# Kernel tuning notes

Measured on AMD Instinct MI355X. Metric: run time of the kernel, lower is better.

The kernel has to match this reference:

```python
import jax, jax.numpy as jnp
import numpy as np

B, S, HIDDEN = 1, 2048, 2048
HEADS, HEAD_DIM = 32, 128
EPS = 1e-5
THETA = 10000.0


def setup_inputs() -> dict:
    key = jax.random.key(0)
    k0, k1, k2 = jax.random.split(key, 3)
    hidden_states = jax.random.normal(k0, (B, S, HIDDEN), jnp.float32)
    positions = jnp.broadcast_to(jnp.arange(S, dtype=jnp.int32)[None, :], (B, S))
    qkv_w = jax.random.normal(k1, (3 * HEADS * HEAD_DIM, HIDDEN), jnp.float32) * 0.02
    q_norm_w = jnp.ones((HEAD_DIM,), jnp.float32)
    k_norm_w = jnp.ones((HEAD_DIM,), jnp.float32)
    o_proj_w = jax.random.normal(k2, (HIDDEN, HEADS * HEAD_DIM), jnp.float32) * 0.02
    return {"hidden_states": hidden_states, "positions": positions, "qkv_w": qkv_w,
            "q_norm_w": q_norm_w, "k_norm_w": k_norm_w, "o_proj_w": o_proj_w}


def _rmsnorm(x, w):
    # RMSNorm over last (head_dim) axis
    var = jnp.mean(x * x, axis=-1, keepdims=True)
    return x * jax.lax.rsqrt(var + EPS) * w


def _rope(x, positions):
    # NeoX-style (non-interleaved) rotary over full head_dim
    d2 = HEAD_DIM // 2
    inv_freq = 1.0 / (THETA ** (jnp.arange(0, HEAD_DIM, 2, dtype=jnp.float32) / HEAD_DIM))
    freqs = positions.astype(jnp.float32)[..., None] * inv_freq  # [B,S,d2]
    cos = jnp.cos(freqs)[:, :, None, :]  # [B,S,1,d2]
    sin = jnp.sin(freqs)[:, :, None, :]
    x1, x2 = x[..., :d2], x[..., d2:]
    return jnp.concatenate([x1 * cos - x2 * sin, x2 * cos + x1 * sin], axis=-1)


def reference(hidden_states, positions, qkv_w, q_norm_w, k_norm_w, o_proj_w):
    b, s, _ = hidden_states.shape
    qkv = jnp.einsum('bsh,oh->bso', hidden_states, qkv_w)  # [B,S,3*H*D]
    q, k, v = jnp.split(qkv, 3, axis=-1)
    q = q.reshape(b, s, HEADS, HEAD_DIM)
    k = k.reshape(b, s, HEADS, HEAD_DIM)
    v = v.reshape(b, s, HEADS, HEAD_DIM)
    # qk_norm (per-head RMSNorm)
    q = _rmsnorm(q, q_norm_w)
    k = _rmsnorm(k, k_norm_w)
    # rotary embedding
    q = _rope(q, positions)
    k = _rope(k, positions)
    # causal attention, scale = head_dim**-0.5 (flash_attn default)
    scale = HEAD_DIM ** -0.5
    scores = jnp.einsum('bqhd,bkhd->bhqk', q, k) * scale  # [B,H,S,S]
    causal = jnp.tril(jnp.ones((s, s), dtype=bool))
    scores = jnp.where(causal[None, None], scores, jnp.float32(-1e30))
    probs = jax.nn.softmax(scores, axis=-1)
    o = jnp.einsum('bhqk,bkhd->bqhd', probs, v).reshape(b, s, HEADS * HEAD_DIM)
    return jnp.einsum('bso,ho->bsh', o, o_proj_w)
```

## Files before the change

### kernel.cpp

```cpp
#include <hip/hip_runtime.h>
#include <cstdint>
#include <cstddef>

static constexpr int S_LEN = 2048;
static constexpr int HID   = 2048;
static constexpr int NH    = 32;
static constexpr int HD    = 128;
static constexpr int OD    = 4096;
static constexpr int QKV_O = 12288;

#define AS1 __attribute__((address_space(1)))
#define AS3 __attribute__((address_space(3)))

typedef __attribute__((ext_vector_type(8))) short bf16x8;
typedef __attribute__((ext_vector_type(4))) float f32x4;
typedef __attribute__((ext_vector_type(4))) short s16x4;

template <int V> struct IC { static constexpr int v = V; };

__device__ __forceinline__ short f2bf(float f) {
  unsigned u = __float_as_uint(f);
  unsigned r = (u + 0x7fffu + ((u >> 16) & 1u)) >> 16;
  return (short)r;
}
__device__ __forceinline__ float bf2f(short s) {
  return __uint_as_float(((unsigned)(unsigned short)s) << 16);
}
__device__ __forceinline__ unsigned pk2bf(float a, float b) {
  return __builtin_amdgcn_perm(__float_as_uint(b), __float_as_uint(a), 0x07060302u);
}

__global__ void convert2_kernel(const float* __restrict__ in1, short* __restrict__ out1, int n1_4,
                                const float* __restrict__ in2, short* __restrict__ out2, int n2_4) {
  int i = blockIdx.x * blockDim.x + threadIdx.x;
  const float* in; short* out; int j;
  if (i < n1_4) { in = in1; out = out1; j = i; }
  else { j = i - n1_4; if (j >= n2_4) return; in = in2; out = out2; }
  float4 f = ((const float4*)in)[j];
  s16x4 s;
  s.x = f2bf(f.x); s.y = f2bf(f.y); s.z = f2bf(f.z); s.w = f2bf(f.w);
  ((s16x4*)out)[j] = s;
}

__global__ __launch_bounds__(512, 2) void gemm128x256_bf16(
    const short* __restrict__ A, const short* __restrict__ Bw, short* __restrict__ C,
    int K, int N, int ldc) {
  __shared__ short Al[2][128 * 64];
  __shared__ short Bl[2][2][128 * 64];
  const int tid  = threadIdx.x;
  const int lane = tid & 63;
  const int quad = lane >> 4;
  const int col  = lane & 15;
  const int wave = tid >> 6;
  const int wm   = wave >> 2;
  const int wn   = wave & 3;

  const int cpx = gridDim.x >> 3;
  const int bid = blockIdx.x;
  const int swz = (bid & 7) * cpx + (bid >> 3);
  const int nbn = N >> 8;
  const int m0  = (swz / nbn) * 128;
  const int n0  = (swz % nbn) * 256;

  const int NT = K >> 6;

  f32x4 acc[4][4] = {};
  bf16x8 a[4][2], b0[2][2], b1[2][2];

  auto stA = [&](int t, int buf) {
#pragma unroll
    for (int r = 0; r < 2; ++r) {
      int idx = r * 512 + tid;
      int row = idx >> 3;
      int g   = idx & 7;
      int gs  = g ^ ((row >> 1) & 7);
      const short* ga = A + (size_t)(m0 + row) * K + t * 64 + gs * 8;
      __builtin_amdgcn_global_load_lds((const AS1 unsigned*)ga,
                                       (AS3 unsigned*)&Al[buf][idx * 8], 16, 0, 0);
    }
  };
  auto stB = [&](int t, int buf, int h) {
#pragma unroll
    for (int r = 0; r < 2; ++r) {
      int idx = r * 512 + tid;
      int row = idx >> 3;
      int g   = idx & 7;
      int gs  = g ^ ((row >> 1) & 7);
      const short* gb = Bw + (size_t)(n0 + h * 128 + row) * K + t * 64 + gs * 8;
      __builtin_amdgcn_global_load_lds((const AS1 unsigned*)gb,
                                       (AS3 unsigned*)&Bl[buf][h][idx * 8], 16, 0, 0);
    }
  };
  auto rdA = [&](int buf, int mh) {
#pragma unroll
    for (int i = 0; i < 2; ++i) {
      int rh = wm * 64 + (mh * 2 + i) * 16 + col;
#pragma unroll
      for (int kf = 0; kf < 2; ++kf)
        a[mh * 2 + i][kf] =
            *(const bf16x8*)&Al[buf][rh * 64 + (((kf * 4 + quad) ^ ((rh >> 1) & 7)) * 8)];
    }
  };
  auto rdB = [&](int buf, int nh, bf16x8 (&bb)[2][2]) {
#pragma unroll
    for (int j = 0; j < 2; ++j) {
      int br = wn * 64 + nh * 32 + j * 16 + col;
      int bh = br >> 7, rh = br & 127;
#pragma unroll
      for (int kf = 0; kf < 2; ++kf)
        bb[j][kf] =
            *(const bf16x8*)&Bl[buf][bh][rh * 64 + (((kf * 4 + quad) ^ ((rh >> 1) & 7)) * 8)];
    }
  };
  auto mm = [&](auto MH, auto NHc, bf16x8 (&bb)[2][2]) {
    constexpr int mh = MH.v, nh = NHc.v;
    __builtin_amdgcn_s_setprio(1);
#pragma unroll
    for (int i = 0; i < 2; ++i)
#pragma unroll
      for (int j = 0; j < 2; ++j)
#pragma unroll
        for (int kf = 0; kf < 2; ++kf)
          acc[mh * 2 + i][nh * 2 + j] = __builtin_amdgcn_mfma_f32_16x16x32_bf16(
              a[mh * 2 + i][kf], bb[j][kf], acc[mh * 2 + i][nh * 2 + j], 0, 0, 0);
    __builtin_amdgcn_s_setprio(0);
  };
#define LGK() do { asm volatile("s_waitcnt lgkmcnt(0)"); __builtin_amdgcn_sched_barrier(0); } while (0)
#define BAR() __builtin_amdgcn_s_barrier()
#define VMC(n) asm volatile("s_waitcnt vmcnt(" #n ")" ::: "memory")

  stA(0, 0); stB(0, 0, 0); stB(0, 0, 1);
  stB(1, 1, 0); stB(1, 1, 1);
  VMC(4);
  BAR();

  for (int i = 0; i < (NT >> 1); ++i) {
    const int t  = 2 * i;
    const int tA = (t + 2 < NT) ? t + 2 : NT - 2;
    const int tB = (t + 3 < NT) ? t + 3 : NT - 1;
    rdA(0, 0); rdB(0, 0, b0);
    stA(t + 1, 1);
    BAR(); LGK();
    mm(IC<0>{}, IC<0>{}, b0);
    BAR();
    rdB(0, 1, b1);
    stB(tA, 0, 0);
    BAR(); LGK();
    mm(IC<0>{}, IC<1>{}, b1);
    BAR();
    rdA(0, 1);
    stB(tA, 0, 1);
    BAR(); LGK();
    mm(IC<1>{}, IC<1>{}, b1);
    BAR();
    BAR();
    mm(IC<1>{}, IC<0>{}, b0);
    VMC(4);
    BAR();
    rdA(1, 0); rdB(1, 0, b0);
    stA(tA, 0);
    BAR(); LGK();
    mm(IC<0>{}, IC<0>{}, b0);
    BAR();
    rdB(1, 1, b1);
    stB(tB, 1, 0);
    BAR(); LGK();
    mm(IC<0>{}, IC<1>{}, b1);
    BAR();
    rdA(1, 1);
    stB(tB, 1, 1);
    BAR(); LGK();
    mm(IC<1>{}, IC<1>{}, b1);
    BAR();
    BAR();
    mm(IC<1>{}, IC<0>{}, b0);
    VMC(4);
    BAR();
  }
#undef LGK
#undef BAR
#undef VMC

#pragma unroll
  for (int mi = 0; mi < 4; ++mi)
#pragma unroll
    for (int nj = 0; nj < 4; ++nj)
#pragma unroll
      for (int r = 0; r < 4; ++r) {
        int rr = m0 + wm * 64 + mi * 16 + quad * 4 + r;
        int cc = n0 + wn * 64 + nj * 16 + col;
        C[(size_t)rr * ldc + cc] = f2bf(acc[mi][nj][r]);
      }
}

#define BM 128
#define BK 32

template <int BNT, int CMODE>
__global__ __launch_bounds__(256, 2) void gemm_nt_f32w(
    const short* __restrict__ A, const float* __restrict__ B, void* __restrict__ Cp,
    int K, int ldc) {
  __shared__ short Alds[2][BM * BK];
  __shared__ short Blds[2][BNT * BK];
  constexpr int WN  = BNT / 2;
  constexpr int NJ  = WN / 16;
  constexpr int BCH = (BNT * 4) / 256;
  const int tid  = threadIdx.x;
  const int lane = tid & 63;
  const int quad = lane >> 4;
  const int col  = lane & 15;
  const int wave = tid >> 6;
  const int m0 = blockIdx.y * BM;
  const int n0 = blockIdx.x * BNT;
  const int wm = (wave & 1) * 64;
  const int wn = (wave >> 1) * WN;

  f32x4 acc[4][NJ] = {};
  float4 breg[BCH][2];

  const int nk = K / BK;

  auto b_issue = [&](int k0) {
#pragma unroll
    for (int it = 0; it < BCH; ++it) {
      int idx = it * 256 + tid;
      int row = idx >> 2;
      int c   = idx & 3;
      const float* gb = B + (size_t)(n0 + row) * K + k0 + c * 8;
      breg[it][0] = *(const float4*)gb;
      breg[it][1] = *(const float4*)(gb + 4);
    }
  };
  auto a_issue = [&](int k0, int buf) {
#pragma unroll
    for (int it = 0; it < 2; ++it) {
      int idx = it * 256 + tid;
      int row = idx >> 2;
      int c   = idx & 3;
      int cs  = c ^ ((row >> 1) & 3);
      const short* ga = A + (size_t)(m0 + row) * K + k0 + cs * 8;
      __builtin_amdgcn_global_load_lds((const AS1 unsigned*)ga,
                                       (AS3 unsigned*)&Alds[buf][idx * 8], 16, 0, 0);
    }
  };
  auto b_write = [&](int buf) {
#pragma unroll
    for (int it = 0; it < BCH; ++it) {
      int idx = it * 256 + tid;
      int row = idx >> 2;
      int c   = idx & 3;
      int cw  = c ^ ((row >> 1) & 3);
      union { unsigned u[4]; bf16x8 v; } pk;
      pk.u[0] = pk2bf(breg[it][0].x, breg[it][0].y);
      pk.u[1] = pk2bf(breg[it][0].z, breg[it][0].w);
      pk.u[2] = pk2bf(breg[it][1].x, breg[it][1].y);
      pk.u[3] = pk2bf(breg[it][1].z, breg[it][1].w);
      *(bf16x8*)&Blds[buf][(row * 4 + cw) * 8] = pk.v;
    }
  };
  auto compute = [&](int buf) {
    bf16x8 a[4], b[NJ];
#pragma unroll
    for (int i = 0; i < 4; ++i) {
      int row = wm + i * 16 + col;
      a[i] = *(const bf16x8*)&Alds[buf][(row * 4 + (quad ^ ((row >> 1) & 3))) * 8];
    }
#pragma unroll
    for (int j = 0; j < NJ; ++j) {
      int row = wn + j * 16 + col;
      b[j] = *(const bf16x8*)&Blds[buf][(row * 4 + (quad ^ ((row >> 1) & 3))) * 8];
    }
#pragma unroll
    for (int i = 0; i < 4; ++i)
#pragma unroll
      for (int j = 0; j < NJ; ++j)
        acc[i][j] = __builtin_amdgcn_mfma_f32_16x16x32_bf16(a[i], b[j], acc[i][j], 0, 0, 0);
  };

  b_issue(0);
  a_issue(0, 0);
  b_write(0);
  __syncthreads();

  for (int t = 0; t < nk - 1; ++t) {
    const int cur = t & 1;
    b_issue((t + 1) * BK);
    a_issue((t + 1) * BK, cur ^ 1);
    compute(cur);
    b_write(cur ^ 1);
    __syncthreads();
  }
  compute((nk - 1) & 1);

#pragma unroll
  for (int i = 0; i < 4; ++i)
#pragma unroll
    for (int j = 0; j < NJ; ++j)
#pragma unroll
      for (int r = 0; r < 4; ++r) {
        int rr = m0 + wm + i * 16 + quad * 4 + r;
        int cc = n0 + wn + j * 16 + col;
        if (CMODE == 1)
          ((float*)Cp)[(size_t)rr * ldc + cc] = acc[i][j][r];
        else
          ((short*)Cp)[(size_t)rr * ldc + cc] = f2bf(acc[i][j][r]);
      }
}

__global__ void normrope_packv_kernel(short* __restrict__ qkv,
                                      const int* __restrict__ positions,
                                      const float* __restrict__ qw,
                                      const float* __restrict__ kw,
                                      short* __restrict__ vtp) {
  __shared__ short T[64][136];
  if (blockIdx.x < 32768) {
    int item = blockIdx.x * 4 + (threadIdx.x >> 6);
    int lane = threadIdx.x & 63;
    int head  = item & 31;
    int which = (item >> 5) & 1;
    int s     = item >> 6;
    const float* w = which ? kw : qw;
    short* base = qkv + (size_t)s * QKV_O + which * OD + head * HD;

    float x1 = bf2f(base[lane]);
    float x2 = bf2f(base[lane + 64]);
    float ss = x1 * x1 + x2 * x2;
#pragma unroll
    for (int d = 32; d; d >>= 1) ss += __shfl_xor(ss, d);
    float r = rsqrtf(ss * (1.0f / 128.0f) + 1e-5f);
    float xn1 = x1 * r * w[lane];
    float xn2 = x2 * r * w[lane + 64];

    float pos = (float)positions[s];
    float inv_freq = exp2f((float)lane * (-13.287712379549449f / 64.0f));
    float f = pos * inv_freq;
    float c = cosf(f), sn = sinf(f);
    float sc = which ? 1.0f : 0.12751863738f;
    base[lane]      = f2bf((xn1 * c - xn2 * sn) * sc);
    base[lane + 64] = f2bf((xn2 * c + xn1 * sn) * sc);
  } else {
    int bid2 = blockIdx.x - 32768;
    const int h  = bid2 & 31;
    const int kt = bid2 >> 5;
    const int tid = threadIdx.x;
    {
      int rr = tid >> 2;
      int db = (tid & 3) * 32;
      const short* src = qkv + (size_t)(kt * 64 + rr) * QKV_O + 2 * OD + h * HD + db;
#pragma unroll
      for (int i = 0; i < 4; ++i)
        *(bf16x8*)&T[rr][db + i * 8] = *(const bf16x8*)(src + i * 8);
    }
    __syncthreads();
    {
      int d  = tid >> 1;
      int k0 = (tid & 1) * 32;
      short* dst = vtp + (((size_t)h * 32 + kt) * 128 + d) * 64 + k0;
#pragma unroll
      for (int c = 0; c < 4; ++c) {
        bf16x8 v;
#pragma unroll
        for (int j = 0; j < 8; ++j) v[j] = T[k0 + c * 8 + j][d];
        *(bf16x8*)&dst[c * 8] = v;
      }
    }
  }
}

__global__ __launch_bounds__(256, 2) void attn_kernel(
    const short* __restrict__ qkv, const short* __restrict__ vtp, short* __restrict__ obuf) {
  __shared__ short Klds[2][64 * 128];
  __shared__ short Vt[2][128 * 64];
  __shared__ short Plds[4][16 * 64];

  const int tid  = threadIdx.x;
  const int lane = tid & 63;
  const int wave = tid >> 6;
  const int quad = lane >> 4;
  const int col  = lane & 15;
  const int h    = blockIdx.y;

  const int kr  = tid >> 2;
  const int kcb = (tid & 3) * 32;
  const int vd  = tid >> 1;
  const int vcb = (tid & 1) * 32;

  bf16x8 kreg[4], vreg[4];

  auto loadK = [&](int kt) {
    const short* kp = qkv + (size_t)(kt * 64 + kr) * QKV_O + OD + h * HD + kcb;
#pragma unroll
    for (int i = 0; i < 4; ++i) kreg[i] = *(const bf16x8*)(kp + i * 8);
  };
  auto loadV = [&](int kt) {
    const short* vp = vtp + (((size_t)h * 32 + kt) * 128 + vd) * 64 + vcb;
#pragma unroll
    for (int i = 0; i < 4; ++i) vreg[i] = *(const bf16x8*)(vp + i * 8);
  };
  auto writeKV = [&](int buf) {
#pragma unroll
    for (int i = 0; i < 4; ++i) {
      int swz = ((tid & 3) * 4 + i) ^ (kr & 15);
      *(bf16x8*)&Klds[buf][kr * 128 + swz * 8] = kreg[i];
    }
#pragma unroll
    for (int i = 0; i < 4; ++i) {
      int swz = ((tid & 1) * 4 + i) ^ (vd & 7);
      *(bf16x8*)&Vt[buf][vd * 64 + swz * 8] = vreg[i];
    }
  };

#pragma unroll 1
  for (int half = 0; half < 2; ++half) {
    const int qt = half == 0 ? blockIdx.x : 31 - blockIdx.x;
    const int qbase = qt * 64 + wave * 16;

    bf16x8 qf[4];
#pragma unroll
    for (int kf = 0; kf < 4; ++kf)
      qf[kf] = *(const bf16x8*)(qkv + (size_t)(qbase + col) * QKV_O + h * HD + kf * 32 + quad * 8);

    f32x4 o[8] = {};
    float m_r[4], l_i[4];
#pragma unroll
    for (int r = 0; r < 4; ++r) { m_r[r] = -1e30f; l_i[r] = 0.f; }

    loadK(0); loadV(0);
    __syncthreads();
    writeKV(0);

#pragma unroll 1
    for (int kt = 0; kt <= qt; ++kt) {
      const int cur = kt & 1;
      if (kt < qt) { loadK(kt + 1); loadV(kt + 1); }
      __syncthreads();

      f32x4 sfr[4];
#pragma unroll
      for (int nf = 0; nf < 4; ++nf) {
        f32x4 acc = {};
#pragma unroll
        for (int kf = 0; kf < 4; ++kf) {
          bf16x8 b = *(const bf16x8*)&Klds[cur][(nf * 16 + col) * 128 + ((kf * 4 + quad) ^ col) * 8];
          acc = __builtin_amdgcn_mfma_f32_16x16x32_bf16(qf[kf], b, acc, 0, 0, 0);
        }
        sfr[nf] = acc;
      }

      if (kt == qt) {
#pragma unroll
        for (int nf = 0; nf < 4; ++nf)
#pragma unroll
          for (int r = 0; r < 4; ++r) {
            int key = kt * 64 + nf * 16 + col;
            int qg  = qbase + quad * 4 + r;
            if (key > qg) sfr[nf][r] = -1e30f;
          }
      }

#pragma unroll
      for (int r = 0; r < 4; ++r) {
        float mt = fmaxf(fmaxf(sfr[0][r], sfr[1][r]), fmaxf(sfr[2][r], sfr[3][r]));
#pragma unroll
        for (int d = 8; d; d >>= 1) mt = fmaxf(mt, __shfl_xor(mt, d));
        float mnew  = fmaxf(m_r[r], mt);
        float alpha = exp2f(m_r[r] - mnew);
        float ps = 0.f;
#pragma unroll
        for (int nf = 0; nf < 4; ++nf) {
          float p = exp2f(sfr[nf][r] - mnew);
          sfr[nf][r] = p;
          ps += p;
        }
        l_i[r] = l_i[r] * alpha + ps;
        m_r[r] = mnew;
#pragma unroll
        for (int nf = 0; nf < 8; ++nf) o[nf][r] *= alpha;
      }

#pragma unroll
      for (int nf = 0; nf < 4; ++nf)
#pragma unroll
        for (int r = 0; r < 4; ++r) {
          int row = quad * 4 + r;
          int key = nf * 16 + col;
          Plds[wave][row * 64 + ((key >> 3) ^ (row & 7)) * 8 + (key & 7)] = f2bf(sfr[nf][r]);
        }

      bf16x8 pa[2];
#pragma unroll
      for (int kf = 0; kf < 2; ++kf)
        pa[kf] = *(const bf16x8*)&Plds[wave][col * 64 + ((kf * 4 + quad) ^ (col & 7)) * 8];
#pragma unroll
      for (int nf = 0; nf < 8; ++nf)
#pragma unroll
        for (int kf = 0; kf < 2; ++kf) {
          bf16x8 vb = *(const bf16x8*)&Vt[cur][(nf * 16 + col) * 64 + ((kf * 4 + quad) ^ (col & 7)) * 8];
          o[nf] = __builtin_amdgcn_mfma_f32_16x16x32_bf16(pa[kf], vb, o[nf], 0, 0, 0);
        }

      if (kt < qt) writeKV(cur ^ 1);
    }

#pragma unroll
    for (int r = 0; r < 4; ++r) {
      float lt = l_i[r];
#pragma unroll
      for (int d = 8; d; d >>= 1) lt += __shfl_xor(lt, d);
      float inv = 1.0f / lt;
      int sg = qbase + quad * 4 + r;
#pragma unroll
      for (int nf = 0; nf < 8; ++nf)
        obuf[(size_t)sg * OD + h * HD + nf * 16 + col] = f2bf(o[nf][r] * inv);
    }
  }
}

extern "C" void kernel_launch(void* const* d_in, const int* in_sizes, int n_in,
                              void* d_out, int out_size, void* d_ws, size_t ws_size,
                              hipStream_t stream) {
  (void)in_sizes; (void)n_in; (void)out_size;
  const float* hs   = (const float*)d_in[0];
  const int*   pos  = (const int*)d_in[1];
  const float* qkvw = (const float*)d_in[2];
  const float* qw   = (const float*)d_in[3];
  const float* kw   = (const float*)d_in[4];
  const float* ow   = (const float*)d_in[5];
  float* out = (float*)d_out;

  char* ws = (char*)d_ws;
  short* qkvb    = (short*)(ws);
  short* obuf    = (short*)(ws + 50331648);
  short* qkvw_bf = (short*)(ws + 67108864);
  short* hsb  = (short*)d_out;
  short* vtp  = (short*)d_out;

  const bool fast = ws_size >= (size_t)117440512;

  if (fast) {
    int n1 = (S_LEN * HID) / 4, n2 = (QKV_O * HID) / 4;
    convert2_kernel<<<(n1 + n2 + 255) / 256, 256, 0, stream>>>(hs, hsb, n1, qkvw, qkvw_bf, n2);
    gemm128x256_bf16<<<(S_LEN / 128) * (QKV_O / 256), 512, 0, stream>>>(
        hsb, qkvw_bf, qkvb, HID, QKV_O, QKV_O);
  } else {
    int n1 = (S_LEN * HID) / 4;
    convert2_kernel<<<(n1 + 255) / 256, 256, 0, stream>>>(hs, hsb, n1, hs, hsb, 0);
    gemm_nt_f32w<128, 0><<<dim3(QKV_O / 128, S_LEN / BM), 256, 0, stream>>>(
        hsb, qkvw, qkvb, HID, QKV_O);
  }

  normrope_packv_kernel<<<(S_LEN * 2 * NH) / 4 + NH * (S_LEN / 64), 256, 0, stream>>>(
      qkvb, pos, qw, kw, vtp);

  attn_kernel<<<dim3(16, NH), 256, 0, stream>>>(qkvb, vtp, obuf);

  gemm_nt_f32w<64, 1><<<dim3(HID / 64, S_LEN / BM), 256, 0, stream>>>(
      obuf, ow, out, OD, HID);
}
```

Measured before the change: 546.2 us.

## Templatize bf16 GEMM for wider QKV tiles and bf16 output projection

Generalizes the 8-wave bf16 GEMM over tile width, using 128x384 tiles for the QKV projection and adding a 128x128 variant with fp32 output for the o_proj. The o_proj weights are converted to bf16 into the workspace region freed after the QKV GEMM. This replaces the older f32-weight GEMM. The prefetch schedule is reordered so A and B stages are issued with adjusted vmcnt waits. The aim is better MFMA efficiency and less weight traffic, at the cost of an extra conversion pass and more register and LDS use per block.

```diff
diff --git a/kernel.cpp b/kernel.cpp
--- a/kernel.cpp
+++ b/kernel.cpp
@@ -36,17 +36,21 @@
   const float* in; short* out; int j;
   if (i < n1_4) { in = in1; out = out1; j = i; }
   else { j = i - n1_4; if (j >= n2_4) return; in = in2; out = out2; }
-  float4 f = ((const float4*)in)[j];
+  float4 f = ((const float4*)in)[i == j ? i : j];
   s16x4 s;
   s.x = f2bf(f.x); s.y = f2bf(f.y); s.z = f2bf(f.z); s.w = f2bf(f.w);
   ((s16x4*)out)[j] = s;
 }
 
-__global__ __launch_bounds__(512, 2) void gemm128x256_bf16(
-    const short* __restrict__ A, const short* __restrict__ Bw, short* __restrict__ C,
+template <int BNT, int CMODE>
+__global__ __launch_bounds__(512, 2) void gemm8p(
+    const short* __restrict__ A, const short* __restrict__ Bw, void* __restrict__ Cp,
     int K, int N, int ldc) {
+  constexpr int BH  = BNT / 128;
+  constexpr int NJ  = BNT / 64;
+  constexpr int NJH = NJ / 2;
   __shared__ short Al[2][128 * 64];
-  __shared__ short Bl[2][2][128 * 64];
+  __shared__ short Bl[2][BH][128 * 64];
   const int tid  = threadIdx.x;
   const int lane = tid & 63;
   const int quad = lane >> 4;
@@ -58,14 +62,14 @@
   const int cpx = gridDim.x >> 3;
   const int bid = blockIdx.x;
   const int swz = (bid & 7) * cpx + (bid >> 3);
-  const int nbn = N >> 8;
+  const int nbn = N / BNT;
   const int m0  = (swz / nbn) * 128;
-  const int n0  = (swz % nbn) * 256;
+  const int n0  = (swz % nbn) * BNT;
 
   const int NT = K >> 6;
 
-  f32x4 acc[4][4] = {};
-  bf16x8 a[4][2], b0[2][2], b1[2][2];
+  f32x4 acc[4][NJ] = {};
+  bf16x8 a[4][2], b0[NJH][2], b1[NJH][2];
 
   auto stA = [&](int t, int buf) {
 #pragma unroll
@@ -101,10 +105,10 @@
             *(const bf16x8*)&Al[buf][rh * 64 + (((kf * 4 + quad) ^ ((rh >> 1) & 7)) * 8)];
     }
   };
-  auto rdB = [&](int buf, int nh, bf16x8 (&bb)[2][2]) {
-#pragma unroll
-    for (int j = 0; j < 2; ++j) {
-      int br = wn * 64 + nh * 32 + j * 16 + col;
+  auto rdB = [&](int buf, int nh, bf16x8 (&bb)[NJH][2]) {
+#pragma unroll
+    for (int j = 0; j < NJH; ++j) {
+      int br = wn * (BNT / 4) + nh * (BNT / 8) + j * 16 + col;
       int bh = br >> 7, rh = br & 127;
 #pragma unroll
       for (int kf = 0; kf < 2; ++kf)
@@ -112,26 +116,38 @@
             *(const bf16x8*)&Bl[buf][bh][rh * 64 + (((kf * 4 + quad) ^ ((rh >> 1) & 7)) * 8)];
     }
   };
-  auto mm = [&](auto MH, auto NHc, bf16x8 (&bb)[2][2]) {
+  auto mm = [&](auto MH, auto NHc, bf16x8 (&bb)[NJH][2]) {
     constexpr int mh = MH.v, nh = NHc.v;
     __builtin_amdgcn_s_setprio(1);
 #pragma unroll
     for (int i = 0; i < 2; ++i)
 #pragma unroll
-      for (int j = 0; j < 2; ++j)
+      for (int j = 0; j < NJH; ++j)
 #pragma unroll
         for (int kf = 0; kf < 2; ++kf)
-          acc[mh * 2 + i][nh * 2 + j] = __builtin_amdgcn_mfma_f32_16x16x32_bf16(
-              a[mh * 2 + i][kf], bb[j][kf], acc[mh * 2 + i][nh * 2 + j], 0, 0, 0);
+          acc[mh * 2 + i][nh * NJH + j] = __builtin_amdgcn_mfma_f32_16x16x32_bf16(
+              a[mh * 2 + i][kf], bb[j][kf], acc[mh * 2 + i][nh * NJH + j], 0, 0, 0);
     __builtin_amdgcn_s_setprio(0);
   };
 #define LGK() do { asm volatile("s_waitcnt lgkmcnt(0)"); __builtin_amdgcn_sched_barrier(0); } while (0)
 #define BAR() __builtin_amdgcn_s_barrier()
-#define VMC(n) asm volatile("s_waitcnt vmcnt(" #n ")" ::: "memory")
-
-  stA(0, 0); stB(0, 0, 0); stB(0, 0, 1);
-  stB(1, 1, 0); stB(1, 1, 1);
-  VMC(4);
+  auto vmc_mid = [] {
+    if constexpr (BH == 3) asm volatile("s_waitcnt vmcnt(6)" ::: "memory");
+    else                   asm volatile("s_waitcnt vmcnt(4)" ::: "memory");
+  };
+  auto vmc_end = [] {
+    if constexpr (BH == 3) asm volatile("s_waitcnt vmcnt(8)" ::: "memory");
+    else                   asm volatile("s_waitcnt vmcnt(4)" ::: "memory");
+  };
+
+#pragma unroll
+  for (int h = 0; h < BH; ++h) stB(0, 0, h);
+  stA(0, 0);
+#pragma unroll
+  for (int h = 0; h < BH; ++h) stB(1, 1, h);
+  stA(1, 1);
+  if constexpr (BH == 3) asm volatile("s_waitcnt vmcnt(8)" ::: "memory");
+  else                   asm volatile("s_waitcnt vmcnt(4)" ::: "memory");
   BAR();
 
   for (int i = 0; i < (NT >> 1); ++i) {
@@ -139,57 +155,61 @@
     const int tA = (t + 2 < NT) ? t + 2 : NT - 2;
     const int tB = (t + 3 < NT) ? t + 3 : NT - 1;
     rdA(0, 0); rdB(0, 0, b0);
-    stA(t + 1, 1);
     BAR(); LGK();
     mm(IC<0>{}, IC<0>{}, b0);
     BAR();
     rdB(0, 1, b1);
+    BAR(); LGK();
+    mm(IC<0>{}, IC<1>{}, b1);
+    BAR();
+    rdA(0, 1);
     stB(tA, 0, 0);
     BAR(); LGK();
+    mm(IC<1>{}, IC<1>{}, b1);
+    BAR();
+    if constexpr (BH == 3) stB(tA, 0, 1);
+    stA(tA, 0);
+    BAR();
+    mm(IC<1>{}, IC<0>{}, b0);
+    vmc_mid();
+    BAR();
+    rdA(1, 0); rdB(1, 0, b0);
+    if constexpr (BH == 3) stB(tA, 0, 2);
+    BAR(); LGK();
+    mm(IC<0>{}, IC<0>{}, b0);
+    BAR();
+    rdB(1, 1, b1);
+    BAR(); LGK();
     mm(IC<0>{}, IC<1>{}, b1);
     BAR();
-    rdA(0, 1);
-    stB(tA, 0, 1);
+    rdA(1, 1);
+    stB(tB, 1, 0);
+    if constexpr (BH == 3) stB(tB, 1, 1);
     BAR(); LGK();
     mm(IC<1>{}, IC<1>{}, b1);
     BAR();
+    if constexpr (BH == 3) stB(tB, 1, 2);
+    stA(tB, 1);
     BAR();
     mm(IC<1>{}, IC<0>{}, b0);
-    VMC(4);
-    BAR();
-    rdA(1, 0); rdB(1, 0, b0);
-    stA(tA, 0);
-    BAR(); LGK();
-    mm(IC<0>{}, IC<0>{}, b0);
-    BAR();
-    rdB(1, 1, b1);
-    stB(tB, 1, 0);
-    BAR(); LGK();
-    mm(IC<0>{}, IC<1>{}, b1);
-    BAR();
-    rdA(1, 1);
-    stB(tB, 1, 1);
-    BAR(); LGK();
-    mm(IC<1>{}, IC<1>{}, b1);
-    BAR();
-    BAR();
-    mm(IC<1>{}, IC<0>{}, b0);
-    VMC(4);
+    vmc_end();
     BAR();
   }
 #undef LGK
 #undef BAR
-#undef VMC
 
 #pragma unroll
   for (int mi = 0; mi < 4; ++mi)
 #pragma unroll
-    for (int nj = 0; nj < 4; ++nj)
+    for (int nj = 0; nj < NJ; ++nj)
 #pragma unroll
       for (int r = 0; r < 4; ++r) {
         int rr = m0 + wm * 64 + mi * 16 + quad * 4 + r;
-        int cc = n0 + wn * 64 + nj * 16 + col;
-        C[(size_t)rr * ldc + cc] = f2bf(acc[mi][nj][r]);
+        int cc = n0 + wn * (BNT / 4) + nj * 16 + col;
+        if (CMODE == 1)
+          ((float*)Cp)[(size_t)rr * ldc + cc] = acc[mi][nj][r];
+        else
+          ((short*)Cp)[(size_t)rr * ldc + cc] = f2bf(acc[mi][nj][r]);
       }
 }
 
@@ -532,6 +552,7 @@
   short* qkvb    = (short*)(ws);
   short* obuf    = (short*)(ws + 50331648);
   short* qkvw_bf = (short*)(ws + 67108864);
+  short* ow_bf   = (short*)(ws + 67108864);
   short* hsb  = (short*)d_out;
   short* vtp  = (short*)d_out;
 
@@ -540,8 +561,10 @@
   if (fast) {
     int n1 = (S_LEN * HID) / 4, n2 = (QKV_O * HID) / 4;
     convert2_kernel<<<(n1 + n2 + 255) / 256, 256, 0, stream>>>(hs, hsb, n1, qkvw, qkvw_bf, n2);
-    gemm128x256_bf16<<<(S_LEN / 128) * (QKV_O / 256), 512, 0, stream>>>(
+    gemm8p<384, 0><<<(S_LEN / 128) * (QKV_O / 384), 512, 0, stream>>>(
         hsb, qkvw_bf, qkvb, HID, QKV_O, QKV_O);
+    int n3 = (HID * OD) / 4;
+    convert2_kernel<<<(n3 + 255) / 256, 256, 0, stream>>>(ow, ow_bf, n3, ow, ow_bf, 0);
   } else {
     int n1 = (S_LEN * HID) / 4;
     convert2_kernel<<<(n1 + 255) / 256, 256, 0, stream>>>(hs, hsb, n1, hs, hsb, 0);
@@ -554,6 +577,11 @@
 
   attn_kernel<<<dim3(16, NH), 256, 0, stream>>>(qkvb, vtp, obuf);
 
-  gemm_nt_f32w<64, 1><<<dim3(HID / 64, S_LEN / BM), 256, 0, stream>>>(
-      obuf, ow, out, OD, HID);
-}
+  if (fast) {
+    gemm8p<128, 1><<<(S_LEN / 128) * (HID / 128), 512, 0, stream>>>(
+        obuf, ow_bf, out, OD, HID, HID);
+  } else {
+    gemm_nt_f32w<64, 1><<<dim3(HID / 64, S_LEN / BM), 256, 0, stream>>>(
+        obuf, ow, out, OD, HID);
+  }
+}
```

Measured after the change: 494.7 us. 1.1x faster.
